# Kernel tuning notes

Hardware: AMD Instinct MI355X
Metric: run time of the kernel (lower is better)

The kernel has to match this reference:

```python
import jax, jax.numpy as jnp
import numpy as np
import random as pyrandom

B, T, D = 2, 2048, 768
H, HD = 12, 64
WINDOW, N_GLOBAL, N_RANDOM, SEED = 64, 32, 16, 0


def _bigbird_mask(Tn, w, g, r, seed):
    # Faithful port of create_bigbird_mask: local band + global rows/cols + random keys
    mask = np.zeros((Tn, Tn), dtype=bool)
    idx = np.arange(Tn)
    mask |= np.abs(idx[None, :] - idx[:, None]) <= w  # local window
    g = min(g, Tn)
    if g > 0:
        mask[:g, :] = True
        mask[:, :g] = True
    if r > 0:
        rng = pyrandom.Random(seed)
        for i in range(g, Tn):
            cand = np.nonzero(~mask[i])[0].tolist()  # same sorted candidate list as torch code
            if cand:
                for j in rng.sample(cand, min(r, len(cand))):
                    mask[i, j] = True
    return jnp.asarray(mask)


def setup_inputs() -> dict:
    key = jax.random.key(0)
    ks = jax.random.split(key, 9)
    s = 1.0 / np.sqrt(D)
    inp = {
        "x": jax.random.normal(ks[0], (B, T, D), dtype=jnp.float32),
        "Wq": jax.random.uniform(ks[1], (D, D), jnp.float32, -s, s),
        "bq": jax.random.uniform(ks[2], (D,), jnp.float32, -s, s),
        "Wk": jax.random.uniform(ks[3], (D, D), jnp.float32, -s, s),
        "bk": jax.random.uniform(ks[4], (D,), jnp.float32, -s, s),
        "Wv": jax.random.uniform(ks[5], (D, D), jnp.float32, -s, s),
        "bv": jax.random.uniform(ks[6], (D,), jnp.float32, -s, s),
        "Wo": jax.random.uniform(ks[7], (D, D), jnp.float32, -s, s),
        "bo": jax.random.uniform(ks[8], (D,), jnp.float32, -s, s),
        "mask": _bigbird_mask(T, WINDOW, N_GLOBAL, N_RANDOM, SEED),
    }
    return inp


def reference(x, Wq, bq, Wk, bk, Wv, bv, Wo, bo, mask):
    Bn, Tn, Dn = x.shape
    scale = HD ** (-0.5)

    def proj(W, b):
        # torch Linear: y = x @ W.T + b ; then split heads -> (B, H, T, HD)
        return (x @ W.T + b).reshape(Bn, Tn, H, HD).transpose(0, 2, 1, 3)

    q, k, v = proj(Wq, bq), proj(Wk, bk), proj(Wv, bv)
    scores = jnp.einsum("bhqd,bhkd->bhqk", q, k) * scale
    scores = jnp.where(mask[None, None], scores, -jnp.inf)
    attn = jnp.nan_to_num(jax.nn.softmax(scores, axis=-1), nan=0.0)
    out = jnp.einsum("bhqk,bhkd->bhqd", attn, v)
    out = out.transpose(0, 2, 1, 3).reshape(Bn, Tn, Dn)
    return out @ Wo.T + bo
```

## Files before the change

kernel.cpp:

```cpp
#include <hip/hip_runtime.h>
#include <hip/hip_bf16.h>
#include <math.h>

#define BB   2
#define TT   2048
#define DD   768
#define HH   12
#define HD   64
#define MM   (BB*TT)
#define BTD  ((long)BB*TT*DD)

typedef __bf16 bf16x8 __attribute__((ext_vector_type(8)));
typedef __bf16 bf16x4 __attribute__((ext_vector_type(4)));
typedef float  f32x4  __attribute__((ext_vector_type(4)));

#define PREP_A 3072
#define PREP_B 2304
#define PREP_C 504

__global__ __launch_bounds__(256) void prep(
    const float* __restrict__ x,
    const float* __restrict__ w0, const float* __restrict__ w1,
    const float* __restrict__ w2, const float* __restrict__ w3,
    const void* __restrict__ maskp,
    __bf16* __restrict__ xb, __bf16* __restrict__ Wcat,
    __bf16* __restrict__ Wob, int* __restrict__ rand_idx)
{
    const int bid = blockIdx.x;
    const int tid = threadIdx.x;

    if (bid < PREP_A) {
        const int i = bid * 256 + tid;
        const float4 v = ((const float4*)x)[i];
        bf16x4 o;
        o.x = (__bf16)v.x; o.y = (__bf16)v.y;
        o.z = (__bf16)v.z; o.w = (__bf16)v.w;
        ((bf16x4*)xb)[i] = o;
        return;
    }
    if (bid < PREP_A + PREP_B) {
        const int idx = bid - PREP_A;
        const int seg = idx / 576;
        const int i = (idx % 576) * 256 + tid;
        const float* src = seg == 0 ? w0 : seg == 1 ? w1 : seg == 2 ? w2 : w3;
        __bf16* dst = seg < 3 ? Wcat + (long)seg * DD * DD : Wob;
        const float4 v = ((const float4*)src)[i];
        bf16x4 o;
        o.x = (__bf16)v.x; o.y = (__bf16)v.y;
        o.z = (__bf16)v.z; o.w = (__bf16)v.w;
        ((bf16x4*)dst)[i] = o;
        return;
    }
    {
        const int cbid = bid - PREP_A - PREP_B;
        const int wid = tid >> 6, lane = tid & 63;
        const int rsel = cbid * 4 + wid;
        if (rsel >= TT - 32) return;
        const int row = 32 + rsel;
        const unsigned char* m8 = (const unsigned char*)maskp;
        const bool u8 = (m8[1] != 0);
        const int c0 = lane * 32;

        unsigned int bits = 0;
        if (u8) {
            const uint4* p = (const uint4*)(m8 + (long)row * TT + c0);
            const uint4 a = p[0], b = p[1];
            const unsigned int wds[8] = {a.x, a.y, a.z, a.w, b.x, b.y, b.z, b.w};
            #pragma unroll
            for (int k = 0; k < 8; k++) {
                const unsigned int w = wds[k];
                bits |= ((w       ) & 1u) << (k * 4 + 0);
                bits |= ((w >>  8 ) & 1u) << (k * 4 + 1);
                bits |= ((w >> 16 ) & 1u) << (k * 4 + 2);
                bits |= ((w >> 24 ) & 1u) << (k * 4 + 3);
            }
        } else {
            const int4* p = (const int4*)((const int*)maskp + (long)row * TT + c0);
            #pragma unroll
            for (int k = 0; k < 8; k++) {
                const int4 v = p[k];
                bits |= (v.x != 0 ? 1u : 0u) << (k * 4 + 0);
                bits |= (v.y != 0 ? 1u : 0u) << (k * 4 + 1);
                bits |= (v.z != 0 ? 1u : 0u) << (k * 4 + 2);
                bits |= (v.w != 0 ? 1u : 0u) << (k * 4 + 3);
            }
        }
        if (lane == 0) bits = 0;
        {
            const int loB = max(row - 64, c0);
            const int hiB = min(row + 64, c0 + 31);
            if (loB <= hiB) {
                const int len = hiB - loB + 1;
                const unsigned int m = (len >= 32) ? 0xFFFFFFFFu
                                                   : (((1u << len) - 1u) << (loB - c0));
                bits &= ~m;
            }
        }

        const int mcnt = __popc(bits);
        int incl = mcnt;
        #pragma unroll
        for (int d = 1; d < 64; d <<= 1) {
            const int n = __shfl_up(incl, d, 64);
            if (lane >= d) incl += n;
        }
        int pos = incl - mcnt;
        unsigned int bb = bits;
        while (bb) {
            const int t = __builtin_ctz(bb);
            bb &= bb - 1;
            if (pos < 16) rand_idx[(long)row * 16 + pos] = c0 + t;
            pos++;
        }
        const int total = __shfl(incl, 63, 64);
        if (lane == 0)
            for (int p = total; p < 16; p++) rand_idx[(long)row * 16 + p] = -1;
    }
}

__global__ __launch_bounds__(256) void mfma_gemm(
    const __bf16* __restrict__ A, const __bf16* __restrict__ Bw,
    const float* __restrict__ b0, const float* __restrict__ b1,
    const float* __restrict__ b2, float* __restrict__ Y,
    __bf16* __restrict__ Yb, __bf16* __restrict__ vTout, int N, int mode)
{
    constexpr int K = DD;
    constexpr int NT = K / 32;
    __shared__ __bf16 As[2][128 * 32];
    __shared__ __bf16 Bs[2][128 * 32];

    const int tid  = threadIdx.x;
    const int wid  = tid >> 6, lane = tid & 63;
    const int fq = lane >> 4, fr = lane & 15;
    const int wr = wid >> 1, wc = wid & 1;

    const int gx = gridDim.x;
    const int nwg = gx * gridDim.y;
    const int bid = blockIdx.y * gx + blockIdx.x;
    const int cpx = nwg >> 3;
    const int swz = (bid & 7) * cpx + (bid >> 3);
    const int m0 = (swz / gx) * 128, n0 = (swz % gx) * 128;

    f32x4 acc[4][4] = {};

    const char* Ag = (const char*)(A + (long)m0 * K);
    const char* Bg = (const char*)(Bw + (long)n0 * K);

    auto stage = [&](int buf, int k0) {
        #pragma unroll
        for (int c = 0; c < 2; c++) {
            const int o   = wid * 2048 + c * 1024 + lane * 16;
            const int row = o >> 6, kb = o & 63;
            const long goff = (long)row * (K * 2) + k0 * 2 + kb;
            __builtin_amdgcn_global_load_lds(
                (const __attribute__((address_space(1))) void*)(Ag + goff),
                (__attribute__((address_space(3))) void*)((char*)As[buf] + wid * 2048 + c * 1024),
                16, 0, 0);
            __builtin_amdgcn_global_load_lds(
                (const __attribute__((address_space(1))) void*)(Bg + goff),
                (__attribute__((address_space(3))) void*)((char*)Bs[buf] + wid * 2048 + c * 1024),
                16, 0, 0);
        }
    };

    auto compute = [&](int buf) {
        bf16x8 af[4], bfr[4];
        #pragma unroll
        for (int m = 0; m < 4; m++)
            af[m] = *(const bf16x8*)(As[buf] + ((wr * 64 + m * 16 + fr) * 32 + fq * 8));
        #pragma unroll
        for (int n = 0; n < 4; n++)
            bfr[n] = *(const bf16x8*)(Bs[buf] + ((wc * 64 + n * 16 + fr) * 32 + fq * 8));
        #pragma unroll
        for (int m = 0; m < 4; m++)
            #pragma unroll
            for (int n = 0; n < 4; n++)
                acc[m][n] = __builtin_amdgcn_mfma_f32_16x16x32_bf16(
                    af[m], bfr[n], acc[m][n], 0, 0, 0);
    };

    int cur = 0;
    stage(0, 0);
    __syncthreads();
    for (int t = 0; t < NT - 1; ++t) {
        stage(cur ^ 1, (t + 1) * 32);
        compute(cur);
        __syncthreads();
        cur ^= 1;
    }
    compute(cur);

    #pragma unroll
    for (int m = 0; m < 4; m++) {
        const int grow = m0 + wr * 64 + m * 16 + fq * 4;
        #pragma unroll
        for (int n = 0; n < 4; n++) {
            const int col = n0 + wc * 64 + n * 16 + fr;
            if (mode == 0) {
                const float bias = b0[col];
                #pragma unroll
                for (int j = 0; j < 4; j++)
                    Y[(long)(grow + j) * N + col] = acc[m][n][j] + bias;
            } else {
                const int which = col / DD;
                const int nn = col - which * DD;
                const float* bp = which == 0 ? b0 : (which == 1 ? b1 : b2);
                const float bias = bp[nn];
                const int h_ = nn >> 6, d_ = nn & 63;
                __bf16* baseb = Yb + (long)which * BTD;
                bf16x4 v4;
                #pragma unroll
                for (int j = 0; j < 4; j++) {
                    const int row = grow + j;
                    const int b_ = row >> 11, t_ = row & (TT - 1);
                    const __bf16 val = (__bf16)(acc[m][n][j] + bias);
                    baseb[(((long)b_ * HH + h_) * TT + t_) * HD + d_] = val;
                    v4[j] = val;
                }
                if (which == 2) {
                    const int b_ = grow >> 11, t0 = grow & (TT - 1);
                    *(bf16x4*)(vTout + (((long)b_ * HH + h_) * HD + d_) * TT + t0) = v4;
                }
            }
        }
    }
}

#define DPROWB 512
#define PROWB 384
#define SW(r) (((r) & 7) << 4)

__global__ __launch_bounds__(256) void bb_attn(
    const __bf16* __restrict__ Qb, const __bf16* __restrict__ Kb,
    const __bf16* __restrict__ Vb, const __bf16* __restrict__ vT,
    const int* __restrict__ rand_idx, float* __restrict__ part,
    __bf16* __restrict__ Ao)
{
    __shared__ __attribute__((aligned(16))) char Pmem[32 * DPROWB];
    __shared__ float Obuf[32][68];
    __shared__ float lbuf[2][32], lrand[32];

    const int bid = blockIdx.x;
    const int tid = threadIdx.x;
    const int w = tid >> 6, lane = tid & 63;
    const int fq = lane >> 4, fr = lane & 15;
    const int qh = w & 1, kr = w >> 1;

    if (bid < 192) {
        const int xcd = bid & 7;
        const int idx = bid >> 3;
        const int gsel = idx >> 3;
        const int ch = idx & 7;
        const int grp = xcd + 8 * gsel;
        const int b = grp / HH, h = grp % HH;
        const int k0 = ch * 256;

        const __bf16* qbase = Qb + ((long)b * HH + h) * TT * HD;
        const __bf16* kbase = Kb + ((long)b * HH + h) * TT * HD;
        const __bf16* vTbase = vT + ((long)b * HH + h) * HD * TT;

        bf16x8 aq[2];
        #pragma unroll
        for (int kk = 0; kk < 2; kk++)
            aq[kk] = *(const bf16x8*)(qbase + (long)(qh * 16 + fr) * HD + kk * 32 + fq * 8);

        f32x4 sc[8];
        #pragma unroll
        for (int t = 0; t < 8; t++) {
            const int key = k0 + (kr * 8 + t) * 16 + fr;
            f32x4 c = {};
            #pragma unroll
            for (int kk = 0; kk < 2; kk++) {
                const bf16x8 bk = *(const bf16x8*)(kbase + (long)key * HD + kk * 32 + fq * 8);
                c = __builtin_amdgcn_mfma_f32_16x16x32_bf16(aq[kk], bk, c, 0, 0, 0);
            }
            sc[t] = c;
        }

        float lsum[4] = {};
        #pragma unroll
        for (int t = 0; t < 8; t++)
            #pragma unroll
            for (int j = 0; j < 4; j++) {
                const float p = __expf(sc[t][j] * 0.125f);
                sc[t][j] = p;
                lsum[j] += p;
            }
        #pragma unroll
        for (int o = 1; o < 16; o <<= 1)
            #pragma unroll
            for (int j = 0; j < 4; j++)
                lsum[j] += __shfl_xor(lsum[j], o, 64);
        if (fr == 0)
            #pragma unroll
            for (int j = 0; j < 4; j++)
                lbuf[kr][qh * 16 + fq * 4 + j] = lsum[j];
        #pragma unroll
        for (int t = 0; t < 8; t++) {
            const int colc = (kr * 8 + t) * 16 + fr;
            #pragma unroll
            for (int j = 0; j < 4; j++) {
                const int rl = qh * 16 + fq * 4 + j;
                *(__bf16*)(Pmem + ((rl * DPROWB + colc * 2) ^ SW(rl))) = (__bf16)sc[t][j];
            }
        }
        __syncthreads();

        f32x4 ov[2] = {};
        {
            const int rl = qh * 16 + fr;
            #pragma unroll
            for (int t = 0; t < 8; t++) {
                const bf16x8 ap = *(const bf16x8*)(Pmem + ((rl * DPROWB + (t * 32 + fq * 8) * 2) ^ SW(rl)));
                #pragma unroll
                for (int ti = 0; ti < 2; ti++) {
                    const int d = kr * 32 + ti * 16 + fr;
                    const bf16x8 bv = *(const bf16x8*)(vTbase + (long)d * TT + k0 + t * 32 + fq * 8);
                    ov[ti] = __builtin_amdgcn_mfma_f32_16x16x32_bf16(ap, bv, ov[ti], 0, 0, 0);
                }
            }
        }

        #pragma unroll
        for (int ti = 0; ti < 2; ti++)
            #pragma unroll
            for (int j = 0; j < 4; j++)
                Obuf[qh * 16 + fq * 4 + j][kr * 32 + ti * 16 + fr] = ov[ti][j];
        __syncthreads();

        {
            const int r = tid >> 3, g = tid & 7;
            float* pb = part + ((((long)b * HH + h) * 8 + ch) * 32 + r) * 66;
            if (g == 0) {
                pb[0] = 0.f;
                pb[1] = lbuf[0][r] + lbuf[1][r];
            }
            #pragma unroll
            for (int e = 0; e < 8; e++)
                pb[2 + g * 8 + e] = Obuf[r][g * 8 + e];
        }
        return;
    }

    const int sbid = bid - 192;
    const int xcd = sbid & 7;
    const int idx = sbid >> 3;
    const int gsel = idx / 63;
    const int tq  = idx % 63;
    const int grp = xcd + 8 * gsel;
    const int b = grp / HH, h = grp % HH;
    const int q0 = (tq + 1) * 32;

    const int lo = max(32, q0 - 64);
    const int hi = min(TT - 1, q0 + 95);

    const __bf16* qbase = Qb + ((long)b * HH + h) * TT * HD;
    const __bf16* kbase = Kb + ((long)b * HH + h) * TT * HD;
    const __bf16* vbase = Vb + ((long)b * HH + h) * TT * HD;
    const __bf16* vTbase = vT + ((long)b * HH + h) * HD * TT;

    const int rr_r = tid >> 3;
    const int g = tid & 7;
    const int grow_r = q0 + rr_r;
    int crand[16];
    {
        const int4* rrv = (const int4*)(rand_idx + (long)grow_r * 16);
        #pragma unroll
        for (int c4 = 0; c4 < 4; c4++) {
            const int4 rv = rrv[c4];
            crand[c4 * 4 + 0] = rv.x; crand[c4 * 4 + 1] = rv.y;
            crand[c4 * 4 + 2] = rv.z; crand[c4 * 4 + 3] = rv.w;
        }
    }

    bf16x8 aq[2];
    #pragma unroll
    for (int kk = 0; kk < 2; kk++)
        aq[kk] = *(const bf16x8*)(qbase + (long)(q0 + qh * 16 + fr) * HD + kk * 32 + fq * 8);

    f32x4 sc[6];
    #pragma unroll
    for (int t6 = 0; t6 < 6; t6++) {
        const int colg = (kr * 6 + t6) * 16 + fr;
        const int keyg = colg < 32 ? colg : lo + colg - 32;
        const int keyc = min(keyg, TT - 1);
        f32x4 c = {};
        #pragma unroll
        for (int kk = 0; kk < 2; kk++) {
            const bf16x8 bk = *(const bf16x8*)(kbase + (long)keyc * HD + kk * 32 + fq * 8);
            c = __builtin_amdgcn_mfma_f32_16x16x32_bf16(aq[kk], bk, c, 0, 0, 0);
        }
        sc[t6] = c;
    }

    float lsum[4] = {};
    #pragma unroll
    for (int t6 = 0; t6 < 6; t6++) {
        const int colg = (kr * 6 + t6) * 16 + fr;
        const int keyg = colg < 32 ? colg : lo + colg - 32;
        #pragma unroll
        for (int j = 0; j < 4; j++) {
            const int grow = q0 + qh * 16 + fq * 4 + j;
            const int dlt = keyg - grow;
            const bool valid = (colg < 32) || (keyg <= hi && dlt <= 64 && dlt >= -64);
            const float p = valid ? __expf(sc[t6][j] * 0.125f) : 0.f;
            sc[t6][j] = p;
            lsum[j] += p;
        }
    }
    #pragma unroll
    for (int o = 1; o < 16; o <<= 1)
        #pragma unroll
        for (int j = 0; j < 4; j++)
            lsum[j] += __shfl_xor(lsum[j], o, 64);
    if (fr == 0)
        #pragma unroll
        for (int j = 0; j < 4; j++)
            lbuf[kr][qh * 16 + fq * 4 + j] = lsum[j];
    #pragma unroll
    for (int t6 = 0; t6 < 6; t6++) {
        const int key = (kr * 6 + t6) * 16 + fr;
        #pragma unroll
        for (int j = 0; j < 4; j++) {
            const int rl = qh * 16 + fq * 4 + j;
            *(__bf16*)(Pmem + ((rl * PROWB + key * 2) ^ SW(rl))) = (__bf16)sc[t6][j];
        }
    }

    const bf16x8 q8 = *(const bf16x8*)(qbase + (long)grow_r * HD + g * 8);
    float srand[16];
    bf16x8 vf0[8];
    #pragma unroll
    for (int j = 0; j < 8; j++)
        vf0[j] = *(const bf16x8*)(vbase + (long)max(crand[j], 0) * HD + g * 8);
    #pragma unroll
    for (int ch = 0; ch < 2; ch++) {
        bf16x8 kf[8];
        #pragma unroll
        for (int j = 0; j < 8; j++)
            kf[j] = *(const bf16x8*)(kbase + (long)max(crand[ch * 8 + j], 0) * HD + g * 8);
        #pragma unroll
        for (int j = 0; j < 8; j++) {
            float s = 0.f;
            #pragma unroll
            for (int e = 0; e < 8; e++) s += (float)q8[e] * (float)kf[j][e];
            s += __shfl_xor(s, 1, 64);
            s += __shfl_xor(s, 2, 64);
            s += __shfl_xor(s, 4, 64);
            srand[ch * 8 + j] = crand[ch * 8 + j] >= 0 ? s * 0.125f : -INFINITY;
        }
    }
    float prand[16];
    {
        float lr = 0.f;
        #pragma unroll
        for (int j = 0; j < 16; j++) {
            prand[j] = __expf(srand[j]);
            lr += prand[j];
        }
        if (g == 0) lrand[rr_r] = lr;
    }

    __syncthreads();

    float arand[8] = {};
    {
        bf16x8 vf1[8];
        #pragma unroll
        for (int j = 0; j < 8; j++)
            vf1[j] = *(const bf16x8*)(vbase + (long)max(crand[8 + j], 0) * HD + g * 8);
        #pragma unroll
        for (int j = 0; j < 8; j++) {
            const float p = prand[j];
            #pragma unroll
            for (int e = 0; e < 8; e++) arand[e] += p * (float)vf0[j][e];
        }
        #pragma unroll
        for (int j = 0; j < 8; j++) {
            const float p = prand[8 + j];
            #pragma unroll
            for (int e = 0; e < 8; e++) arand[e] += p * (float)vf1[j][e];
        }
    }

    f32x4 ov[2] = {};
    {
        const int rl = qh * 16 + fr;
        #pragma unroll
        for (int t = 0; t < 6; t++) {
            const bf16x8 ap = *(const bf16x8*)(Pmem + ((rl * PROWB + (t * 32 + fq * 8) * 2) ^ SW(rl)));
            const int key0 = t * 32 + fq * 8;
            int tg = key0 < 32 ? key0 : lo + key0 - 32;
            tg = min(tg, TT - 8);
            #pragma unroll
            for (int ti = 0; ti < 2; ti++) {
                const int d = kr * 32 + ti * 16 + fr;
                const bf16x8 bv = *(const bf16x8*)(vTbase + (long)d * TT + tg);
                ov[ti] = __builtin_amdgcn_mfma_f32_16x16x32_bf16(ap, bv, ov[ti], 0, 0, 0);
            }
        }
    }

    #pragma unroll
    for (int ti = 0; ti < 2; ti++)
        #pragma unroll
        for (int j = 0; j < 4; j++)
            Obuf[qh * 16 + fq * 4 + j][kr * 32 + ti * 16 + fr] = ov[ti][j];

    __syncthreads();

    {
        const float linv = 1.f /
            (lbuf[0][rr_r] + lbuf[1][rr_r] + lrand[rr_r]);
        bf16x8 o8;
        #pragma unroll
        for (int e = 0; e < 8; e++)
            o8[e] = (__bf16)((Obuf[rr_r][g * 8 + e] + arand[e]) * linv);
        *(bf16x8*)(Ao + ((long)b * TT + grow_r) * DD + h * HD + g * 8) = o8;
    }
}

__global__ __launch_bounds__(256) void bb_dense_combine(
    const float* __restrict__ part, __bf16* __restrict__ Ao)
{
    const int h = blockIdx.x, b = blockIdx.y;
    const int tid = threadIdx.x;
    const int r = tid >> 3, dsl = (tid & 7) * 8;
    const float* pb = part + (((long)b * HH + h) * 8 * 32 + r) * 66;
    float M = -INFINITY;
    #pragma unroll
    for (int c = 0; c < 8; c++) M = fmaxf(M, pb[(long)c * 32 * 66]);
    float L = 0.f, o[8] = {};
    #pragma unroll
    for (int c = 0; c < 8; c++) {
        const float* pc = pb + (long)c * 32 * 66;
        const float w = __expf(pc[0] - M);
        L += w * pc[1];
        #pragma unroll
        for (int j = 0; j < 8; j++) o[j] += w * pc[2 + dsl + j];
    }
    const float inv = 1.f / L;
    const long ob = ((long)b * TT + r) * DD + h * HD + dsl;
    #pragma unroll
    for (int j = 0; j < 8; j++) Ao[ob + j] = (__bf16)(o[j] * inv);
}

extern "C" void kernel_launch(void* const* d_in, const int* in_sizes, int n_in,
                              void* d_out, int out_size, void* d_ws, size_t ws_size,
                              hipStream_t stream)
{
    const float* x  = (const float*)d_in[0];
    const float* Wq = (const float*)d_in[1];
    const float* bq = (const float*)d_in[2];
    const float* Wk = (const float*)d_in[3];
    const float* bk = (const float*)d_in[4];
    const float* Wv = (const float*)d_in[5];
    const float* bv = (const float*)d_in[6];
    const float* Wo = (const float*)d_in[7];
    const float* bo = (const float*)d_in[8];
    const void*  mask = d_in[9];

    __bf16* xb   = (__bf16*)d_ws;
    __bf16* qkvb = xb + BTD;
    __bf16* vTb  = qkvb + 3 * BTD;
    __bf16* aob  = vTb + BTD;
    __bf16* Wcat = aob + BTD;
    __bf16* Wob  = Wcat + (long)3 * DD * DD;
    int*    rand_idx = (int*)(Wob + (long)DD * DD);
    float*  part = (float*)(rand_idx + (long)TT * 16);

    prep<<<PREP_A + PREP_B + PREP_C, 256, 0, stream>>>(
        x, Wq, Wk, Wv, Wo, mask, xb, Wcat, Wob, rand_idx);

    mfma_gemm<<<dim3(3 * DD / 128, MM / 128), 256, 0, stream>>>(
        xb, Wcat, bq, bk, bv, nullptr, qkvb, vTb, 3 * DD, 1);

    bb_attn<<<192 + 1512, 256, 0, stream>>>(
        qkvb, qkvb + BTD, qkvb + 2 * BTD, vTb, rand_idx, part, aob);

    bb_dense_combine<<<dim3(HH, BB), 256, 0, stream>>>(part, aob);

    mfma_gemm<<<dim3(DD / 128, MM / 128), 256, 0, stream>>>(
        aob, Wob, bo, bo, bo, (float*)d_out, nullptr, nullptr, DD, 0);
}
```

Before: 113.9 us.

## Cut registers and LDS in bb_attn to raise occupancy

Adds a launch bound of 8 blocks per CU to bb_attn and drops the separate Obuf shared array, reusing the P buffer (Pmem) for the output tile behind an extra barrier. The random-key path now handles keys in chunks of four, rereading the indices from global memory, and passes the softmax weights through a small shared array instead of holding 16 K/V fragments and probabilities in registers. The goal is lower VGPR and LDS use per block so more waves fit on a CU. The cost is extra syncs, repeated index loads and less in-flight memory parallelism per thread; the forced bound could also cause spills.

```diff
diff --git a/kernel.cpp b/kernel.cpp
--- a/kernel.cpp
+++ b/kernel.cpp
@@ -230,15 +230,15 @@
 #define PROWB 384
 #define SW(r) (((r) & 7) << 4)
 
-__global__ __launch_bounds__(256) void bb_attn(
+__global__ __launch_bounds__(256, 8) void bb_attn(
     const __bf16* __restrict__ Qb, const __bf16* __restrict__ Kb,
     const __bf16* __restrict__ Vb, const __bf16* __restrict__ vT,
     const int* __restrict__ rand_idx, float* __restrict__ part,
     __bf16* __restrict__ Ao)
 {
     __shared__ __attribute__((aligned(16))) char Pmem[32 * DPROWB];
-    __shared__ float Obuf[32][68];
     __shared__ float lbuf[2][32], lrand[32];
+    __shared__ float prl[32][16];
 
     const int bid = blockIdx.x;
     const int tid = threadIdx.x;
@@ -320,12 +320,14 @@
                 }
             }
         }
-
+        __syncthreads();
+
+        float* Ob = (float*)Pmem;
         #pragma unroll
         for (int ti = 0; ti < 2; ti++)
             #pragma unroll
             for (int j = 0; j < 4; j++)
-                Obuf[qh * 16 + fq * 4 + j][kr * 32 + ti * 16 + fr] = ov[ti][j];
+                Ob[(qh * 16 + fq * 4 + j) * 68 + kr * 32 + ti * 16 + fr] = ov[ti][j];
         __syncthreads();
 
         {
@@ -337,7 +339,7 @@
             }
             #pragma unroll
             for (int e = 0; e < 8; e++)
-                pb[2 + g * 8 + e] = Obuf[r][g * 8 + e];
+                pb[2 + g * 8 + e] = Ob[r * 68 + g * 8 + e];
         }
         return;
     }
@@ -362,16 +364,7 @@
     const int rr_r = tid >> 3;
     const int g = tid & 7;
     const int grow_r = q0 + rr_r;
-    int crand[16];
-    {
-        const int4* rrv = (const int4*)(rand_idx + (long)grow_r * 16);
-        #pragma unroll
-        for (int c4 = 0; c4 < 4; c4++) {
-            const int4 rv = rrv[c4];
-            crand[c4 * 4 + 0] = rv.x; crand[c4 * 4 + 1] = rv.y;
-            crand[c4 * 4 + 2] = rv.z; crand[c4 * 4 + 3] = rv.w;
-        }
-    }
+    const int4* rrp = (const int4*)(rand_idx + (long)grow_r * 16);
 
     bf16x8 aq[2];
     #pragma unroll
@@ -427,36 +420,29 @@
         }
     }
 
-    const bf16x8 q8 = *(const bf16x8*)(qbase + (long)grow_r * HD + g * 8);
-    float srand[16];
-    bf16x8 vf0[8];
-    #pragma unroll
-    for (int j = 0; j < 8; j++)
-        vf0[j] = *(const bf16x8*)(vbase + (long)max(crand[j], 0) * HD + g * 8);
-    #pragma unroll
-    for (int ch = 0; ch < 2; ch++) {
-        bf16x8 kf[8];
-        #pragma unroll
-        for (int j = 0; j < 8; j++)
-            kf[j] = *(const bf16x8*)(kbase + (long)max(crand[ch * 8 + j], 0) * HD + g * 8);
-        #pragma unroll
-        for (int j = 0; j < 8; j++) {
-            float s = 0.f;
-            #pragma unroll
-            for (int e = 0; e < 8; e++) s += (float)q8[e] * (float)kf[j][e];
-            s += __shfl_xor(s, 1, 64);
-            s += __shfl_xor(s, 2, 64);
-            s += __shfl_xor(s, 4, 64);
-            srand[ch * 8 + j] = crand[ch * 8 + j] >= 0 ? s * 0.125f : -INFINITY;
-        }
-    }
-    float prand[16];
     {
+        const bf16x8 q8 = *(const bf16x8*)(qbase + (long)grow_r * HD + g * 8);
         float lr = 0.f;
         #pragma unroll
-        for (int j = 0; j < 16; j++) {
-            prand[j] = __expf(srand[j]);
-            lr += prand[j];
+        for (int ch = 0; ch < 4; ch++) {
+            const int4 rv = rrp[ch];
+            const int cr[4] = {rv.x, rv.y, rv.z, rv.w};
+            bf16x8 kf[4];
+            #pragma unroll
+            for (int j = 0; j < 4; j++)
+                kf[j] = *(const bf16x8*)(kbase + (long)max(cr[j], 0) * HD + g * 8);
+            #pragma unroll
+            for (int j = 0; j < 4; j++) {
+                float s = 0.f;
+                #pragma unroll
+                for (int e = 0; e < 8; e++) s += (float)q8[e] * (float)kf[j][e];
+                s += __shfl_xor(s, 1, 64);
+                s += __shfl_xor(s, 2, 64);
+                s += __shfl_xor(s, 4, 64);
+                const float p = (cr[j] >= 0) ? __expf(s * 0.125f) : 0.f;
+                if (g == 0) prl[rr_r][ch * 4 + j] = p;
+                lr += p;
+            }
         }
         if (g == 0) lrand[rr_r] = lr;
     }
@@ -464,22 +450,19 @@
     __syncthreads();
 
     float arand[8] = {};
-    {
-        bf16x8 vf1[8];
-        #pragma unroll
-        for (int j = 0; j < 8; j++)
-            vf1[j] = *(const bf16x8*)(vbase + (long)max(crand[8 + j], 0) * HD + g * 8);
-        #pragma unroll
-        for (int j = 0; j < 8; j++) {
-            const float p = prand[j];
-            #pragma unroll
-            for (int e = 0; e < 8; e++) arand[e] += p * (float)vf0[j][e];
-        }
-        #pragma unroll
-        for (int j = 0; j < 8; j++) {
-            const float p = prand[8 + j];
-            #pragma unroll
-            for (int e = 0; e < 8; e++) arand[e] += p * (float)vf1[j][e];
+    #pragma unroll
+    for (int ch = 0; ch < 4; ch++) {
+        const int4 rv = rrp[ch];
+        const int cr[4] = {rv.x, rv.y, rv.z, rv.w};
+        bf16x8 vf[4];
+        #pragma unroll
+        for (int j = 0; j < 4; j++)
+            vf[j] = *(const bf16x8*)(vbase + (long)max(cr[j], 0) * HD + g * 8);
+        #pragma unroll
+        for (int j = 0; j < 4; j++) {
+            const float p = prl[rr_r][ch * 4 + j];
+            #pragma unroll
+            for (int e = 0; e < 8; e++) arand[e] += p * (float)vf[j][e];
         }
     }
 
@@ -500,12 +483,14 @@
             }
         }
     }
-
+    __syncthreads();
+
+    float* Ob = (float*)Pmem;
     #pragma unroll
     for (int ti = 0; ti < 2; ti++)
         #pragma unroll
         for (int j = 0; j < 4; j++)
-            Obuf[qh * 16 + fq * 4 + j][kr * 32 + ti * 16 + fr] = ov[ti][j];
+            Ob[(qh * 16 + fq * 4 + j) * 68 + kr * 32 + ti * 16 + fr] = ov[ti][j];
 
     __syncthreads();
 
@@ -515,7 +500,7 @@
         bf16x8 o8;
         #pragma unroll
         for (int e = 0; e < 8; e++)
-            o8[e] = (__bf16)((Obuf[rr_r][g * 8 + e] + arand[e]) * linv);
+            o8[e] = (__bf16)((Ob[rr_r * 68 + g * 8 + e] + arand[e]) * linv);
         *(bf16x8*)(Ao + ((long)b * TT + grow_r) * DD + h * HD + g * 8) = o8;
     }
 }
```

New measurement: 121.3 us. +6.5%, slower.
